# Kernel tuning notes

Hardware: AMD Instinct MI355X
Metric: run time of the kernel (lower is better)

## Reference

```python
import jax, jax.numpy as jnp
import numpy as np

B, L, HS = 2, 2048, 2048
NH, NKV, HD = 16, 4, 128
EPS = 1e-6
ROPE_BASE = 10000.0
SCALE = HD ** -0.5


def setup_inputs() -> dict:
    key = jax.random.key(0)
    ks = jax.random.split(key, 5)
    w = lambda k, shape: (jax.random.normal(k, shape, jnp.float32) * 0.02)
    return {
        "hidden_states": jax.random.normal(ks[0], (B, L, HS), jnp.float32),
        "Wq": w(ks[1], (HS, NH * HD)),
        "Wk": w(ks[2], (HS, NKV * HD)),
        "Wv": w(ks[3], (HS, NKV * HD)),
        "Wo": w(ks[4], (NH * HD, HS)),
        "q_norm_w": jnp.ones((HD,), jnp.float32),
        "k_norm_w": jnp.ones((HD,), jnp.float32),
    }


def _rmsnorm(x, w):
    return x * jax.lax.rsqrt(jnp.mean(x * x, axis=-1, keepdims=True) + EPS) * w


def _rope(x, cos, sin):
    # x: [B, L, heads, HD]; cos/sin: [1, L, 1, HD//2]
    x1, x2 = jnp.split(x, 2, axis=-1)
    return jnp.concatenate([x1 * cos - x2 * sin, x2 * cos + x1 * sin], axis=-1)


def reference(hidden_states, Wq, Wk, Wv, Wo, q_norm_w, k_norm_w):
    b, l, _ = hidden_states.shape
    n_rep = NH // NKV
    q = (hidden_states @ Wq).reshape(b, l, NH, HD)
    k = (hidden_states @ Wk).reshape(b, l, NKV, HD)
    v = (hidden_states @ Wv).reshape(b, l, NKV, HD)
    # QK RMSNorm over head_dim
    q = _rmsnorm(q, q_norm_w)
    k = _rmsnorm(k, k_norm_w)
    # RoPE with position_ids = arange(L)
    pos = jnp.arange(l, dtype=jnp.float32)
    inv_freq = 1.0 / (ROPE_BASE ** (jnp.arange(0, HD, 2, dtype=jnp.float32) / HD))
    ang = pos[:, None] * inv_freq  # [L, HD//2]
    cos = jnp.cos(ang)[None, :, None, :]
    sin = jnp.sin(ang)[None, :, None, :]
    q = _rope(q, cos, sin)
    k = _rope(k, cos, sin)
    # GQA: torch expand+reshape gives q head h -> kv head (h mod NKV);
    # reshape q to [B, L, n_rep, NKV, HD] (h = r*NKV + j) and contract per kv group.
    qg = q.reshape(b, l, n_rep, NKV, HD)
    scores = jnp.einsum("blrjd,bmjd->brjlm", qg, k) * SCALE  # [B, r, j, L, L]
    causal = jnp.tril(jnp.ones((l, l), dtype=bool))
    scores = jnp.where(causal, scores, -jnp.inf)
    probs = jax.nn.softmax(scores, axis=-1)
    out = jnp.einsum("brjlm,bmjd->blrjd", probs, v).reshape(b, l, NH * HD)
    return out @ Wo
```

## Files before the change

kernel.cpp:

```cpp
#include <hip/hip_runtime.h>
#include <hip/hip_bf16.h>

#define B_  2
#define L_  2048
#define HS_ 2048
#define NH_ 16
#define NKV_ 4
#define HD_ 128
#define EPS_ 1e-6f
#define SCALE_ 0.08838834764831843f
#define LOG2E_ 1.4426950408889634f

typedef __attribute__((ext_vector_type(8))) short bf16x8;
typedef __attribute__((ext_vector_type(4))) float f32x4;

__device__ __forceinline__ f32x4 mfma16(bf16x8 a, bf16x8 b, f32x4 c) {
    return __builtin_amdgcn_mfma_f32_16x16x32_bf16(a, b, c, 0, 0, 0);
}

__device__ __forceinline__ void async_copy16(void* lds, const void* g) {
    __builtin_amdgcn_global_load_lds(
        (const __attribute__((address_space(1))) unsigned int*)g,
        (__attribute__((address_space(3))) unsigned int*)lds,
        16, 0, 0);
}

__device__ __forceinline__ unsigned cvtpk(float lo, float hi) {
    unsigned r;
    asm("v_cvt_pk_bf16_f32 %0, %1, %2" : "=v"(r) : "v"(lo), "v"(hi));
    return r;
}

__global__ __launch_bounds__(256) void cvt_f32_bf16(const float* __restrict__ src,
                                                    __hip_bfloat16* __restrict__ dst,
                                                    int n4) {
    int i = blockIdx.x * 256 + threadIdx.x;
    if (i >= n4) return;
    float4 v = ((const float4*)src)[i];
    union { __hip_bfloat16 h[4]; short4 s; } u;
    u.h[0] = __float2bfloat16(v.x);
    u.h[1] = __float2bfloat16(v.y);
    u.h[2] = __float2bfloat16(v.z);
    u.h[3] = __float2bfloat16(v.w);
    ((short4*)dst)[i] = u.s;
}

__global__ __launch_bounds__(256) void transpose_cvt(const float* __restrict__ src,
                                                     __hip_bfloat16* __restrict__ dst,
                                                     int K, int N) {
    __shared__ float tile[32][33];
    int n0 = blockIdx.x * 32, k0 = blockIdx.y * 32;
    int tx = threadIdx.x & 31, ty = threadIdx.x >> 5;
#pragma unroll
    for (int i = 0; i < 32; i += 8)
        tile[ty + i][tx] = src[(size_t)(k0 + ty + i) * N + n0 + tx];
    __syncthreads();
#pragma unroll
    for (int i = 0; i < 32; i += 8)
        dst[(size_t)(n0 + ty + i) * K + k0 + tx] = __float2bfloat16(tile[tx][ty + i]);
}

__global__ __launch_bounds__(256) void v_transpose(const float* __restrict__ KV,
                                                   __hip_bfloat16* __restrict__ Vt) {
    __shared__ float tile[32][33];
    int bkv = blockIdx.z;
    int b = bkv >> 2, kv = bkv & 3;
    int l0 = blockIdx.x * 32, d0 = blockIdx.y * 32;
    int tx = threadIdx.x & 31, ty = threadIdx.x >> 5;
#pragma unroll
    for (int i = 0; i < 32; i += 8)
        tile[ty + i][tx] = KV[(size_t)(b * L_ + l0 + ty + i) * 1024 + 512 + kv * HD_ + d0 + tx];
    __syncthreads();
#pragma unroll
    for (int i = 0; i < 32; i += 8)
        Vt[((size_t)(b * NKV_ + kv) * HD_ + d0 + ty + i) * L_ + l0 + tx] =
            __float2bfloat16(tile[tx][ty + i]);
}

#define GNT 32
#define GKB 4096
__global__ __launch_bounds__(512, 2) void gemm8_bf16(const __hip_bfloat16* __restrict__ A,
                                                     const __hip_bfloat16* __restrict__ Bt,
                                                     float* __restrict__ C1,
                                                     float* __restrict__ C2,
                                                     int Ntot, int splitN) {
    __shared__ __align__(16) char lds[131072];
    int t = threadIdx.x;
    int w = t >> 6, lane = t & 63;
    int row16 = lane & 15, quad = lane >> 4, e7 = row16 & 7;
    int wr = w >> 2, wc = w & 3;

    int gx = gridDim.x;
    int nwg = gx * gridDim.y;
    int bid = blockIdx.y * gx + blockIdx.x;
    int cpx = nwg >> 3;
    int swz = (bid & 7) * cpx + (bid >> 3);
    int bx = swz % gx, by = swz / gx;
    int m0 = bx * 256, n0 = by * 256;

    const char* baseA[2];
    const char* baseB[2];
#pragma unroll
    for (int kc = 0; kc < 2; ++kc) {
        int so = ((kc * 4 + quad) ^ e7) << 4;
        baseA[kc] = lds + wr * 16384 + row16 * 128 + so;
        baseB[kc] = lds + 65536 + wc * 8192 + row16 * 128 + so;
    }

    int r8 = lane >> 3;
    int sl = (lane & 7) ^ r8;
    char* dstA = lds + wr * 16384 + (w & 3) * 2048 + lane * 16;
    char* dstB = lds + 65536 + (w >> 1) * 8192 + (w & 1) * 2048 + lane * 16;
    const char* gA = (const char*)A +
        (size_t)(m0 + wr * 128 + (w & 3) * 16 + r8) * GKB + sl * 16;
    const char* gB = (const char*)Bt +
        (size_t)(n0 + (w >> 1) * 64 + (w & 1) * 16 + r8) * GKB + sl * 16;

    f32x4 acc[8][4] = {};
    bf16x8 a[4][2], b[2][2];

#pragma unroll
    for (int i = 0; i < 2; ++i) async_copy16(dstA + i * 1024, gA + i * 32768);
#pragma unroll
    for (int i = 0; i < 2; ++i) async_copy16(dstB + i * 1024, gB + i * 32768);
#pragma unroll
    for (int i = 0; i < 2; ++i) async_copy16(dstB + 4096 + i * 1024, gB + 131072 + i * 32768);
#pragma unroll
    for (int i = 0; i < 2; ++i) async_copy16(dstA + 8192 + i * 1024, gA + 262144 + i * 32768);

    for (int Tb = 0; Tb < GNT; Tb += 2) {
#pragma unroll
        for (int u = 0; u < 2; ++u) {
            const int T = Tb + u;
            const int cu = u * 32768, du = (u ^ 1) * 32768;
            const int tn = (T + 1 < GNT ? T + 1 : T) * 128;

            asm volatile("s_waitcnt vmcnt(4)" ::: "memory");
            __builtin_amdgcn_s_barrier();
            __builtin_amdgcn_sched_barrier(0);
#pragma unroll
            for (int mi = 0; mi < 4; ++mi)
#pragma unroll
                for (int kc = 0; kc < 2; ++kc)
                    a[mi][kc] = *(const bf16x8*)(baseA[kc] + cu + mi * 2048);
#pragma unroll
            for (int ni = 0; ni < 2; ++ni)
#pragma unroll
                for (int kc = 0; kc < 2; ++kc)
                    b[ni][kc] = *(const bf16x8*)(baseB[kc] + cu + ni * 2048);
#pragma unroll
            for (int i = 0; i < 2; ++i)
                async_copy16(dstA + du + i * 1024, gA + tn + i * 32768);
            asm volatile("s_waitcnt lgkmcnt(0)" ::: "memory");
            __builtin_amdgcn_sched_barrier(0);
            __builtin_amdgcn_s_setprio(1);
#pragma unroll
            for (int mi = 0; mi < 4; ++mi)
#pragma unroll
                for (int ni = 0; ni < 2; ++ni)
#pragma unroll
                    for (int kc = 0; kc < 2; ++kc)
                        acc[mi][ni] = mfma16(a[mi][kc], b[ni][kc], acc[mi][ni]);
            __builtin_amdgcn_s_setprio(0);

            asm volatile("s_waitcnt vmcnt(4)" ::: "memory");
            __builtin_amdgcn_s_barrier();
            __builtin_amdgcn_sched_barrier(0);
#pragma unroll
            for (int ni = 0; ni < 2; ++ni)
#pragma unroll
                for (int kc = 0; kc < 2; ++kc)
                    b[ni][kc] = *(const bf16x8*)(baseB[kc] + cu + 4096 + ni * 2048);
#pragma unroll
            for (int i = 0; i < 2; ++i)
                async_copy16(dstB + du + i * 1024, gB + tn + i * 32768);
            asm volatile("s_waitcnt lgkmcnt(0)" ::: "memory");
            __builtin_amdgcn_sched_barrier(0);
            __builtin_amdgcn_s_setprio(1);
#pragma unroll
            for (int mi = 0; mi < 4; ++mi)
#pragma unroll
                for (int ni = 0; ni < 2; ++ni)
#pragma unroll
                    for (int kc = 0; kc < 2; ++kc)
                        acc[mi][2 + ni] = mfma16(a[mi][kc], b[ni][kc], acc[mi][2 + ni]);
            __builtin_amdgcn_s_setprio(0);

            asm volatile("s_waitcnt vmcnt(4)" ::: "memory");
            __builtin_amdgcn_s_barrier();
            __builtin_amdgcn_sched_barrier(0);
#pragma unroll
            for (int mi = 0; mi < 4; ++mi)
#pragma unroll
                for (int kc = 0; kc < 2; ++kc)
                    a[mi][kc] = *(const bf16x8*)(baseA[kc] + cu + 8192 + mi * 2048);
#pragma unroll
            for (int i = 0; i < 2; ++i)
                async_copy16(dstB + du + 4096 + i * 1024, gB + 131072 + tn + i * 32768);
            asm volatile("s_waitcnt lgkmcnt(0)" ::: "memory");
            __builtin_amdgcn_sched_barrier(0);
            __builtin_amdgcn_s_setprio(1);
#pragma unroll
            for (int mi = 0; mi < 4; ++mi)
#pragma unroll
                for (int ni = 0; ni < 2; ++ni)
#pragma unroll
                    for (int kc = 0; kc < 2; ++kc)
                        acc[4 + mi][2 + ni] = mfma16(a[mi][kc], b[ni][kc], acc[4 + mi][2 + ni]);
            __builtin_amdgcn_s_setprio(0);

            __builtin_amdgcn_s_barrier();
            __builtin_amdgcn_sched_barrier(0);
#pragma unroll
            for (int ni = 0; ni < 2; ++ni)
#pragma unroll
                for (int kc = 0; kc < 2; ++kc)
                    b[ni][kc] = *(const bf16x8*)(baseB[kc] + cu + ni * 2048);
#pragma unroll
            for (int i = 0; i < 2; ++i)
                async_copy16(dstA + du + 8192 + i * 1024, gA + 262144 + tn + i * 32768);
            asm volatile("s_waitcnt lgkmcnt(0)" ::: "memory");
            __builtin_amdgcn_sched_barrier(0);
            __builtin_amdgcn_s_setprio(1);
#pragma unroll
            for (int mi = 0; mi < 4; ++mi)
#pragma unroll
                for (int ni = 0; ni < 2; ++ni)
#pragma unroll
                    for (int kc = 0; kc < 2; ++kc)
                        acc[4 + mi][ni] = mfma16(a[mi][kc], b[ni][kc], acc[4 + mi][ni]);
            __builtin_amdgcn_s_setprio(0);
        }
    }

    float* Cb; int cs, ccol0;
    if (n0 < splitN) { Cb = C1; cs = splitN; ccol0 = n0; }
    else             { Cb = C2; cs = Ntot - splitN; ccol0 = n0 - splitN; }
#pragma unroll
    for (int mi = 0; mi < 8; ++mi)
#pragma unroll
        for (int ni = 0; ni < 4; ++ni) {
            int rbase = m0 + wr * 128 + mi * 16 + quad * 4;
            int col = ccol0 + wc * 64 + ni * 16 + row16;
#pragma unroll
            for (int r = 0; r < 4; ++r)
                Cb[(size_t)(rbase + r) * cs + col] = acc[mi][ni][r];
        }
}

__global__ __launch_bounds__(512, 2) void gemm_o(const __hip_bfloat16* __restrict__ A,
                                                 const __hip_bfloat16* __restrict__ Bt,
                                                 float* __restrict__ C) {
    __shared__ __align__(16) char lds[98304];
    int t = threadIdx.x;
    int w = t >> 6, lane = t & 63;
    int row16 = lane & 15, quad = lane >> 4, e7 = row16 & 15 & 7;
    int wr = w >> 2, wc = w & 3;

    int gx = gridDim.x;
    int nwg = gx * gridDim.y;
    int bid = blockIdx.y * gx + blockIdx.x;
    int cpx = nwg >> 3;
    int swz = (bid & 7) * cpx + (bid >> 3);
    int bx = swz % gx, by = swz / gx;
    int m0 = bx * 128, n0 = by * 256;

    const char* baseA[2];
    const char* baseB[2];
#pragma unroll
    for (int kc = 0; kc < 2; ++kc) {
        int so = ((kc * 4 + quad) ^ e7) << 4;
        baseA[kc] = lds + wr * 8192 + row16 * 128 + so;
        baseB[kc] = lds + 32768 + wc * 8192 + row16 * 128 + so;
    }

    int r8 = lane >> 3;
    int sl = (lane & 7) ^ r8;
    int arow_lo = ((w & 4) << 4) + (w & 3) * 8;
    int li0 = w * 2;
    int brow_lo0 = ((li0) >> 2) * 64 + ((li0) & 3) * 8;
    int brow_lo1 = ((li0 + 1) >> 2) * 64 + ((li0 + 1) & 3) * 8;

    char* dAlo = lds + arow_lo * 128 + lane * 16;
    char* dBlo0 = lds + 32768 + brow_lo0 * 128 + lane * 16;
    char* dBlo1 = lds + 32768 + brow_lo1 * 128 + lane * 16;
    const char* gAlo = (const char*)A + (size_t)(m0 + arow_lo + r8) * GKB + sl * 16;
    const char* gBlo0 = (const char*)Bt + (size_t)(n0 + brow_lo0 + r8) * GKB + sl * 16;
    const char* gBlo1 = (const char*)Bt + (size_t)(n0 + brow_lo1 + r8) * GKB + sl * 16;
    const int HI_L = 32 * 128;
    const size_t HI_G = (size_t)32 * GKB;

    f32x4 acc[4][4] = {};
    bf16x8 a[2][2], b[2][2];

    async_copy16(dAlo, gAlo);
    async_copy16(dBlo0, gBlo0);
    async_copy16(dBlo1, gBlo1);
    async_copy16(dBlo0 + HI_L, gBlo0 + HI_G);
    async_copy16(dBlo1 + HI_L, gBlo1 + HI_G);
    async_copy16(dAlo + HI_L, gAlo + HI_G);

    for (int Tb = 0; Tb < GNT; Tb += 2) {
#pragma unroll
        for (int u = 0; u < 2; ++u) {
            const int T = Tb + u;
            const int cuA = u * 16384, duA = (u ^ 1) * 16384;
            const int cuB = u * 32768, duB = (u ^ 1) * 32768;
            const int tn = (T + 1 < GNT ? T + 1 : T) * 128;

            asm volatile("s_waitcnt vmcnt(3)" ::: "memory");
            __builtin_amdgcn_s_barrier();
            __builtin_amdgcn_sched_barrier(0);
#pragma unroll
            for (int mi = 0; mi < 2; ++mi)
#pragma unroll
                for (int kc = 0; kc < 2; ++kc)
                    a[mi][kc] = *(const bf16x8*)(baseA[kc] + cuA + mi * 2048);
#pragma unroll
            for (int ni = 0; ni < 2; ++ni)
#pragma unroll
                for (int kc = 0; kc < 2; ++kc)
                    b[ni][kc] = *(const bf16x8*)(baseB[kc] + cuB + ni * 2048);
            async_copy16(dAlo + duA, gAlo + tn);
            asm volatile("s_waitcnt lgkmcnt(0)" ::: "memory");
            __builtin_amdgcn_sched_barrier(0);
            __builtin_amdgcn_s_setprio(1);
#pragma unroll
            for (int mi = 0; mi < 2; ++mi)
#pragma unroll
                for (int ni = 0; ni < 2; ++ni)
#pragma unroll
                    for (int kc = 0; kc < 2; ++kc)
                        acc[mi][ni] = mfma16(a[mi][kc], b[ni][kc], acc[mi][ni]);
            __builtin_amdgcn_s_setprio(0);

            asm volatile("s_waitcnt vmcnt(2)" ::: "memory");
            __builtin_amdgcn_s_barrier();
            __builtin_amdgcn_sched_barrier(0);
#pragma unroll
            for (int ni = 0; ni < 2; ++ni)
#pragma unroll
                for (int kc = 0; kc < 2; ++kc)
                    b[ni][kc] = *(const bf16x8*)(baseB[kc] + cuB + 4096 + ni * 2048);
            async_copy16(dBlo0 + duB, gBlo0 + tn);
            async_copy16(dBlo1 + duB, gBlo1 + tn);
            asm volatile("s_waitcnt lgkmcnt(0)" ::: "memory");
            __builtin_amdgcn_sched_barrier(0);
            __builtin_amdgcn_s_setprio(1);
#pragma unroll
            for (int mi = 0; mi < 2; ++mi)
#pragma unroll
                for (int ni = 0; ni < 2; ++ni)
#pragma unroll
                    for (int kc = 0; kc < 2; ++kc)
                        acc[mi][2 + ni] = mfma16(a[mi][kc], b[ni][kc], acc[mi][2 + ni]);
            __builtin_amdgcn_s_setprio(0);

            asm volatile("s_waitcnt vmcnt(3)" ::: "memory");
            __builtin_amdgcn_s_barrier();
            __builtin_amdgcn_sched_barrier(0);
#pragma unroll
            for (int mi = 0; mi < 2; ++mi)
#pragma unroll
                for (int kc = 0; kc < 2; ++kc)
                    a[mi][kc] = *(const bf16x8*)(baseA[kc] + cuA + 4096 + mi * 2048);
            async_copy16(dBlo0 + HI_L + duB, gBlo0 + HI_G + tn);
            async_copy16(dBlo1 + HI_L + duB, gBlo1 + HI_G + tn);
            asm volatile("s_waitcnt lgkmcnt(0)" ::: "memory");
            __builtin_amdgcn_sched_barrier(0);
            __builtin_amdgcn_s_setprio(1);
#pragma unroll
            for (int mi = 0; mi < 2; ++mi)
#pragma unroll
                for (int ni = 0; ni < 2; ++ni)
#pragma unroll
                    for (int kc = 0; kc < 2; ++kc)
                        acc[2 + mi][2 + ni] = mfma16(a[mi][kc], b[ni][kc], acc[2 + mi][2 + ni]);
            __builtin_amdgcn_s_setprio(0);

            __builtin_amdgcn_s_barrier();
            __builtin_amdgcn_sched_barrier(0);
#pragma unroll
            for (int ni = 0; ni < 2; ++ni)
#pragma unroll
                for (int kc = 0; kc < 2; ++kc)
                    b[ni][kc] = *(const bf16x8*)(baseB[kc] + cuB + ni * 2048);
            async_copy16(dAlo + HI_L + duA, gAlo + HI_G + tn);
            asm volatile("s_waitcnt lgkmcnt(0)" ::: "memory");
            __builtin_amdgcn_sched_barrier(0);
            __builtin_amdgcn_s_setprio(1);
#pragma unroll
            for (int mi = 0; mi < 2; ++mi)
#pragma unroll
                for (int ni = 0; ni < 2; ++ni)
#pragma unroll
                    for (int kc = 0; kc < 2; ++kc)
                        acc[2 + mi][ni] = mfma16(a[mi][kc], b[ni][kc], acc[2 + mi][ni]);
            __builtin_amdgcn_s_setprio(0);
        }
    }
    asm volatile("s_waitcnt vmcnt(0)" ::: "memory");

#pragma unroll
    for (int mi = 0; mi < 4; ++mi)
#pragma unroll
        for (int ni = 0; ni < 4; ++ni) {
            int rbase = m0 + wr * 64 + mi * 16 + quad * 4;
            int col = n0 + wc * 64 + ni * 16 + row16;
#pragma unroll
            for (int r = 0; r < 4; ++r)
                C[(size_t)(rbase + r) * 2048 + col] = acc[mi][ni][r];
        }
}

__global__ __launch_bounds__(256) void norm_rope(const float* __restrict__ X,
                                                 __hip_bfloat16* __restrict__ Y,
                                                 const float* __restrict__ w,
                                                 int log2nh, int in_stride, float oscale) {
    int row = blockIdx.x * 4 + (threadIdx.x >> 6);
    int lane = threadIdx.x & 63;
    int m = row >> log2nh;
    int head = row & ((1 << log2nh) - 1);
    int pos = m & (L_ - 1);
    const float* x = X + (size_t)m * in_stride + head * HD_;
    float x1 = x[lane], x2 = x[lane + 64];
    float ss = x1 * x1 + x2 * x2;
#pragma unroll
    for (int mm = 1; mm < 64; mm <<= 1) ss += __shfl_xor(ss, mm);
    float rms = rsqrtf(ss * (1.0f / 128.0f) + EPS_);
    float xn1 = x1 * rms * w[lane];
    float xn2 = x2 * rms * w[lane + 64];
    float inv_freq = __builtin_exp2f(-(float)lane * 0.20762050593046014f);
    float ang = (float)pos * inv_freq;
    float c = cosf(ang), s = sinf(ang);
    __hip_bfloat16* y = Y + (size_t)row * HD_;
    y[lane]      = __float2bfloat16((xn1 * c - xn2 * s) * oscale);
    y[lane + 64] = __float2bfloat16((xn2 * c + xn1 * s) * oscale);
}

__global__ __launch_bounds__(256, 2) void flash_attn(const __hip_bfloat16* __restrict__ Q,
                                                     const __hip_bfloat16* __restrict__ Kb,
                                                     const __hip_bfloat16* __restrict__ Vt,
                                                     __hip_bfloat16* __restrict__ O) {
    __shared__ __align__(16) __hip_bfloat16 sK[2][64 * 128];
    __shared__ __align__(16) __hip_bfloat16 sV[2][128 * 64];
    __shared__ __align__(16) __hip_bfloat16 sP[4][16 * 72];

    int t = threadIdx.x, wave = t >> 6, lane = t & 63;
    int row16 = lane & 15, quad = lane >> 4;
    int h = blockIdx.y, b = blockIdx.z;
    int kv = h & (NKV_ - 1);
    int x = blockIdx.x;
    int qtA = x, qtB = 31 - x;
    int nA = qtA + 1;
    const int nTot = 33;

    int e7 = row16 & 7;
    int kOff[4], vOff[2];
#pragma unroll
    for (int kc = 0; kc < 4; ++kc)
        kOff[kc] = row16 * 256 + (((kc * 4 + quad) ^ e7) * 16);
#pragma unroll
    for (int kc2 = 0; kc2 < 2; ++kc2)
        vOff[kc2] = row16 * 128 + (((kc2 * 4 + quad) ^ e7) * 16);

    const char* sKb = (const char*)&sK[0][0];
    const char* sVb = (const char*)&sV[0][0];
    char* myP = (char*)&sP[wave][0];
    int pW = row16 * 144 + quad * 8;
    int pR = row16 * 144 + quad * 16;

    const char* gK[4];
    const char* gV[4];
#pragma unroll
    for (int i = 0; i < 4; ++i) {
        int rk = wave * 16 + i * 4 + quad;
        int ck = row16 ^ (rk & 7);
        gK[i] = (const char*)(Kb + ((size_t)(b * L_ + rk) * NKV_ + kv) * HD_ + ck * 8);
        int rv = wave * 32 + i * 8 + (lane >> 3);
        int cv = (lane & 7) ^ (rv & 7);
        gV[i] = (const char*)(Vt + ((size_t)(b * NKV_ + kv) * HD_ + rv) * L_ + cv * 8);
    }
    char* dK = (char*)&sK[0][0] + wave * 4096 + lane * 16;
    char* dV = (char*)&sV[0][0] + wave * 4096 + lane * 16;

    bf16x8 qf[4];
    f32x4 accO[8];
    float lrow;
    int q0w = 0;

    auto loadQ = [&](int qt) {
        q0w = qt * 64 + wave * 16;
        const __hip_bfloat16* qbase =
            Q + ((size_t)(b * L_ + q0w + row16) * NH_ + h) * HD_ + quad * 8;
#pragma unroll
        for (int kc = 0; kc < 4; ++kc) qf[kc] = *(const bf16x8*)(qbase + kc * 32);
#pragma unroll
        for (int db = 0; db < 8; ++db) accO[db] = f32x4{0.f, 0.f, 0.f, 0.f};
        lrow = 0.f;
    };

    auto epilogue = [&]() {
        float l = lrow;
        l += __shfl_xor(l, 16);
        l += __shfl_xor(l, 32);
        float linv = 1.0f / l;
        __hip_bfloat16* obase = O + ((size_t)(b * L_ + q0w + row16) * NH_ + h) * HD_;
#pragma unroll
        for (int db = 0; db < 8; ++db) {
            union { __hip_bfloat16 h4[4]; short4 s4; } u;
#pragma unroll
            for (int r = 0; r < 4; ++r) u.h4[r] = __float2bfloat16(accO[db][r] * linv);
            *(short4*)(obase + db * 16 + quad * 4) = u.s4;
        }
    };

    auto stage = [&](int s1) {
        int kb64 = (s1 < nA ? s1 : s1 - nA) * 64;
        int buf = (s1 & 1) * 16384;
        int ko = kb64 * 1024;
        int vo = kb64 * 2;
#pragma unroll
        for (int i = 0; i < 4; ++i) {
            async_copy16(dK + buf + i * 1024, gK[i] + ko);
            async_copy16(dV + buf + i * 1024, gV[i] + vo);
        }
    };

    loadQ(qtA);
    stage(0);
    for (int s = 0; s < nTot; ++s) {
        __syncthreads();
        if (s + 1 < nTot) stage(s + 1);
        if (s == nA) { epilogue(); loadQ(qtB); }
        int kcur = (s < nA ? s : s - nA) * 64;
        const char* cK = sKb + (s & 1) * 16384;
        const char* cV = sVb + (s & 1) * 16384;

        f32x4 st[4];
        __builtin_amdgcn_s_setprio(1);
#pragma unroll
        for (int kb = 0; kb < 4; ++kb) {
            f32x4 acc = {};
#pragma unroll
            for (int kc = 0; kc < 4; ++kc) {
                bf16x8 kf = *(const bf16x8*)(cK + kb * 4096 + kOff[kc]);
                acc = mfma16(kf, qf[kc], acc);
            }
            st[kb] = acc;
        }
        __builtin_amdgcn_s_setprio(0);

        float p[4][4];
        if (kcur + 63 > q0w) {
            int qgRel = q0w + row16 - kcur - quad * 4;
#pragma unroll
            for (int kb = 0; kb < 4; ++kb)
#pragma unroll
                for (int r = 0; r < 4; ++r) {
                    float e = __builtin_exp2f(st[kb][r]);
                    p[kb][r] = (kb * 16 + r <= qgRel) ? e : 0.f;
                }
        } else {
#pragma unroll
            for (int kb = 0; kb < 4; ++kb)
#pragma unroll
                for (int r = 0; r < 4; ++r)
                    p[kb][r] = __builtin_exp2f(st[kb][r]);
        }
#pragma unroll
        for (int kb = 0; kb < 4; ++kb)
#pragma unroll
            for (int r = 0; r < 4; ++r) lrow += p[kb][r];

#pragma unroll
        for (int kb = 0; kb < 4; ++kb) {
            uint2 u;
            u.x = cvtpk(p[kb][0], p[kb][1]);
            u.y = cvtpk(p[kb][2], p[kb][3]);
            *(uint2*)(myP + pW + kb * 32) = u;
        }
        asm volatile("s_waitcnt lgkmcnt(0)" ::: "memory");
        bf16x8 pf[2];
        pf[0] = *(const bf16x8*)(myP + pR);
        pf[1] = *(const bf16x8*)(myP + pR + 64);

        __builtin_amdgcn_s_setprio(1);
#pragma unroll
        for (int db = 0; db < 8; ++db) {
#pragma unroll
            for (int kc2 = 0; kc2 < 2; ++kc2) {
                bf16x8 vf = *(const bf16x8*)(cV + db * 2048 + vOff[kc2]);
                accO[db] = mfma16(vf, pf[kc2], accO[db]);
            }
        }
        __builtin_amdgcn_s_setprio(0);
    }
    epilogue();
}

extern "C" void kernel_launch(void* const* d_in, const int* in_sizes, int n_in,
                              void* d_out, int out_size, void* d_ws, size_t ws_size,
                              hipStream_t stream) {
    const float* hidden = (const float*)d_in[0];
    const float* Wq = (const float*)d_in[1];
    const float* Wk = (const float*)d_in[2];
    const float* Wv = (const float*)d_in[3];
    const float* Wo = (const float*)d_in[4];
    const float* qw = (const float*)d_in[5];
    const float* kw = (const float*)d_in[6];
    float* out = (float*)d_out;

    char* ws = (char*)d_ws;
    size_t off = 0;
    auto alloc = [&](size_t bytes) { char* p = ws + off; off += (bytes + 255) & ~255ull; return p; };
    __hip_bfloat16* Wq_t = (__hip_bfloat16*)alloc((size_t)HS_ * NH_ * HD_ * 2);
    __hip_bfloat16* Wk_t = (__hip_bfloat16*)alloc((size_t)HS_ * NKV_ * HD_ * 2);
    __hip_bfloat16* Wv_t = (__hip_bfloat16*)alloc((size_t)HS_ * NKV_ * HD_ * 2);
    __hip_bfloat16* Wo_t = (__hip_bfloat16*)alloc((size_t)HS_ * NH_ * HD_ * 2);
    __hip_bfloat16* A_h  = (__hip_bfloat16*)alloc((size_t)B_ * L_ * HS_ * 2);
    float* kv_f32 = (float*)alloc((size_t)B_ * L_ * 1024 * 4);
    __hip_bfloat16* q_bf  = (__hip_bfloat16*)alloc((size_t)B_ * L_ * NH_ * HD_ * 2);
    __hip_bfloat16* k_bf  = (__hip_bfloat16*)alloc((size_t)B_ * L_ * NKV_ * HD_ * 2);
    __hip_bfloat16* vt_bf = (__hip_bfloat16*)alloc((size_t)B_ * NKV_ * HD_ * L_ * 2);
    float* q_f32 = out;
    __hip_bfloat16* attn_bf = A_h;

    const int M = B_ * L_;

    cvt_f32_bf16<<<(M * HS_ / 4 + 255) / 256, 256, 0, stream>>>(hidden, A_h, M * HS_ / 4);
    transpose_cvt<<<dim3(2048 / 32, 2048 / 32), 256, 0, stream>>>(Wq, Wq_t, HS_, 2048);
    transpose_cvt<<<dim3(512 / 32, 2048 / 32), 256, 0, stream>>>(Wk, Wk_t, HS_, 512);
    transpose_cvt<<<dim3(512 / 32, 2048 / 32), 256, 0, stream>>>(Wv, Wv_t, HS_, 512);
    transpose_cvt<<<dim3(2048 / 32, 2048 / 32), 256, 0, stream>>>(Wo, Wo_t, HS_, 2048);
    gemm8_bf16<<<dim3(M / 256, 3072 / 256), 512, 0, stream>>>(
        A_h, Wq_t, q_f32, kv_f32, 3072, 2048);
    norm_rope<<<(M * NH_) / 4, 256, 0, stream>>>(q_f32, q_bf, qw, 4, 2048, SCALE_ * LOG2E_);
    norm_rope<<<(M * NKV_) / 4, 256, 0, stream>>>(kv_f32, k_bf, kw, 2, 1024, 1.0f);
    v_transpose<<<dim3(L_ / 32, HD_ / 32, B_ * NKV_), 256, 0, stream>>>(kv_f32, vt_bf);
    flash_attn<<<dim3(16, NH_, B_), 256, 0, stream>>>(q_bf, k_bf, vt_bf, attn_bf);
    gemm_o<<<dim3(M / 128, 2048 / 256), 512, 0, stream>>>(attn_bf, Wo_t, out);
}
```

Baseline: 303.7 us.

## Process two 16-row query groups per wave in flash attention with 128-thread blocks

Each wave now handles 32 query rows (two 16-row MFMA groups) instead of 16, and the block shrinks from four waves to two while keeping a 64-row query tile. K and V fragments read from LDS are reused across both query groups, halving LDS read traffic per MFMA. Each wave issues twice as many async K/V copies to fill the same tiles. The cost is doubled accumulator registers per thread and fewer resident waves per CU for latency hiding.

New measurement: 321.3 us. 5.8% more time.

```diff
diff --git a/kernel.cpp b/kernel.cpp
--- a/kernel.cpp
+++ b/kernel.cpp
@@ -438,13 +438,13 @@
     y[lane + 64] = __float2bfloat16((xn2 * c + xn1 * s) * oscale);
 }
 
-__global__ __launch_bounds__(256, 2) void flash_attn(const __hip_bfloat16* __restrict__ Q,
+__global__ __launch_bounds__(128, 1) void flash_attn(const __hip_bfloat16* __restrict__ Q,
                                                      const __hip_bfloat16* __restrict__ Kb,
                                                      const __hip_bfloat16* __restrict__ Vt,
                                                      __hip_bfloat16* __restrict__ O) {
     __shared__ __align__(16) __hip_bfloat16 sK[2][64 * 128];
     __shared__ __align__(16) __hip_bfloat16 sV[2][128 * 64];
-    __shared__ __align__(16) __hip_bfloat16 sP[4][16 * 72];
+    __shared__ __align__(16) __hip_bfloat16 sP[2][16 * 72];
 
     int t = threadIdx.x, wave = t >> 6, lane = t & 63;
     int row16 = lane & 15, quad = lane >> 4;
@@ -470,48 +470,55 @@
     int pW = row16 * 144 + quad * 8;
     int pR = row16 * 144 + quad * 16;
 
-    const char* gK[4];
-    const char* gV[4];
-#pragma unroll
-    for (int i = 0; i < 4; ++i) {
-        int rk = wave * 16 + i * 4 + quad;
+    const char* gK[8];
+    const char* gV[8];
+#pragma unroll
+    for (int i = 0; i < 8; ++i) {
+        int rk = wave * 32 + i * 4 + quad;
         int ck = row16 ^ (rk & 7);
         gK[i] = (const char*)(Kb + ((size_t)(b * L_ + rk) * NKV_ + kv) * HD_ + ck * 8);
-        int rv = wave * 32 + i * 8 + (lane >> 3);
+        int rv = wave * 64 + i * 8 + (lane >> 3);
         int cv = (lane & 7) ^ (rv & 7);
         gV[i] = (const char*)(Vt + ((size_t)(b * NKV_ + kv) * HD_ + rv) * L_ + cv * 8);
     }
-    char* dK = (char*)&sK[0][0] + wave * 4096 + lane * 16;
-    char* dV = (char*)&sV[0][0] + wave * 4096 + lane * 16;
-
-    bf16x8 qf[4];
-    f32x4 accO[8];
-    float lrow;
+    char* dK = (char*)&sK[0][0] + wave * 8192 + lane * 16;
+    char* dV = (char*)&sV[0][0] + wave * 8192 + lane * 16;
+
+    bf16x8 qf[2][4];
+    f32x4 accO[2][8];
+    float lrow[2];
     int q0w = 0;
 
     auto loadQ = [&](int qt) {
-        q0w = qt * 64 + wave * 16;
-        const __hip_bfloat16* qbase =
-            Q + ((size_t)(b * L_ + q0w + row16) * NH_ + h) * HD_ + quad * 8;
-#pragma unroll
-        for (int kc = 0; kc < 4; ++kc) qf[kc] = *(const bf16x8*)(qbase + kc * 32);
-#pragma unroll
-        for (int db = 0; db < 8; ++db) accO[db] = f32x4{0.f, 0.f, 0.f, 0.f};
-        lrow = 0.f;
+        q0w = qt * 64 + wave * 32;
+#pragma unroll
+        for (int qg = 0; qg < 2; ++qg) {
+            const __hip_bfloat16* qbase =
+                Q + ((size_t)(b * L_ + q0w + qg * 16 + row16) * NH_ + h) * HD_ + quad * 8;
+#pragma unroll
+            for (int kc = 0; kc < 4; ++kc) qf[qg][kc] = *(const bf16x8*)(qbase + kc * 32);
+#pragma unroll
+            for (int db = 0; db < 8; ++db) accO[qg][db] = f32x4{0.f, 0.f, 0.f, 0.f};
+            lrow[qg] = 0.f;
+        }
     };
 
     auto epilogue = [&]() {
-        float l = lrow;
-        l += __shfl_xor(l, 16);
-        l += __shfl_xor(l, 32);
-        float linv = 1.0f / l;
-        __hip_bfloat16* obase = O + ((size_t)(b * L_ + q0w + row16) * NH_ + h) * HD_;
-#pragma unroll
-        for (int db = 0; db < 8; ++db) {
-            union { __hip_bfloat16 h4[4]; short4 s4; } u;
-#pragma unroll
-            for (int r = 0; r < 4; ++r) u.h4[r] = __float2bfloat16(accO[db][r] * linv);
-            *(short4*)(obase + db * 16 + quad * 4) = u.s4;
+#pragma unroll
+        for (int qg = 0; qg < 2; ++qg) {
+            float l = lrow[qg];
+            l += __shfl_xor(l, 16);
+            l += __shfl_xor(l, 32);
+            float linv = 1.0f / l;
+            __hip_bfloat16* obase =
+                O + ((size_t)(b * L_ + q0w + qg * 16 + row16) * NH_ + h) * HD_;
+#pragma unroll
+            for (int db = 0; db < 8; ++db) {
+                union { __hip_bfloat16 h4[4]; short4 s4; } u;
+#pragma unroll
+                for (int r = 0; r < 4; ++r) u.h4[r] = __float2bfloat16(accO[qg][db][r] * linv);
+                *(short4*)(obase + db * 16 + quad * 4) = u.s4;
+            }
         }
     };
 
@@ -521,7 +528,7 @@
         int ko = kb64 * 1024;
         int vo = kb64 * 2;
 #pragma unroll
-        for (int i = 0; i < 4; ++i) {
+        for (int i = 0; i < 8; ++i) {
             async_copy16(dK + buf + i * 1024, gK[i] + ko);
             async_copy16(dV + buf + i * 1024, gV[i] + vo);
         }
@@ -537,53 +544,75 @@
         const char* cK = sKb + (s & 1) * 16384;
         const char* cV = sVb + (s & 1) * 16384;
 
-        f32x4 st[4];
+        f32x4 st[2][4];
         __builtin_amdgcn_s_setprio(1);
 #pragma unroll
         for (int kb = 0; kb < 4; ++kb) {
-            f32x4 acc = {};
-#pragma unroll
-            for (int kc = 0; kc < 4; ++kc) {
-                bf16x8 kf = *(const bf16x8*)(cK + kb * 4096 + kOff[kc]);
-                acc = mfma16(kf, qf[kc], acc);
+            bf16x8 kf[4];
+#pragma unroll
+            for (int kc = 0; kc < 4; ++kc)
+                kf[kc] = *(const bf16x8*)(cK + kb * 4096 + kOff[kc]);
+#pragma unroll
+            for (int qg = 0; qg < 2; ++qg) {
+                f32x4 acc = {};
+#pragma unroll
+                for (int kc = 0; kc < 4; ++kc)
+                    acc = mfma16(kf[kc], qf[qg][kc], acc);
+                st[qg][kb] = acc;
             }
-            st[kb] = acc;
         }
         __builtin_amdgcn_s_setprio(0);
 
-        float p[4][4];
+        float p[2][4][4];
         if (kcur + 63 > q0w) {
-            int qgRel = q0w + row16 - kcur - quad * 4;
+#pragma unroll
+            for (int qg = 0; qg < 2; ++qg) {
+                int qgRel = q0w + qg * 16 + row16 - kcur - quad * 4;
+#pragma unroll
+                for (int kb = 0; kb < 4; ++kb)
+#pragma unroll
+                    for (int r = 0; r < 4; ++r) {
+                        float e = __builtin_exp2f(st[qg][kb][r]);
+                        p[qg][kb][r] = (kb * 16 + r <= qgRel) ? e : 0.f;
+                    }
+            }
+        } else {
+#pragma unroll
+            for (int qg = 0; qg < 2; ++qg)
+#pragma unroll
+                for (int kb = 0; kb < 4; ++kb)
+#pragma unroll
+                    for (int r = 0; r < 4; ++r)
+                        p[qg][kb][r] = __builtin_exp2f(st[qg][kb][r]);
+        }
+#pragma unroll
+        for (int qg = 0; qg < 2; ++qg)
 #pragma unroll
             for (int kb = 0; kb < 4; ++kb)
 #pragma unroll
-                for (int r = 0; r < 4; ++r) {
-                    float e = __builtin_exp2f(st[kb][r]);
-                    p[kb][r] = (kb * 16 + r <= qgRel) ? e : 0.f;
-                }
-        } else {
-#pragma unroll
-            for (int kb = 0; kb < 4; ++kb)
-#pragma unroll
-                for (int r = 0; r < 4; ++r)
-                    p[kb][r] = __builtin_exp2f(st[kb][r]);
-        }
-#pragma unroll
-        for (int kb = 0; kb < 4; ++kb)
-#pragma unroll
-            for (int r = 0; r < 4; ++r) lrow += p[kb][r];
-
+                for (int r = 0; r < 4; ++r) lrow[qg] += p[qg][kb][r];
+
+        bf16x8 pf0[2], pf1[2];
 #pragma unroll
         for (int kb = 0; kb < 4; ++kb) {
             uint2 u;
-            u.x = cvtpk(p[kb][0], p[kb][1]);
-            u.y = cvtpk(p[kb][2], p[kb][3]);
+            u.x = cvtpk(p[0][kb][0], p[0][kb][1]);
+            u.y = cvtpk(p[0][kb][2], p[0][kb][3]);
             *(uint2*)(myP + pW + kb * 32) = u;
         }
         asm volatile("s_waitcnt lgkmcnt(0)" ::: "memory");
-        bf16x8 pf[2];
-        pf[0] = *(const bf16x8*)(myP + pR);
-        pf[1] = *(const bf16x8*)(myP + pR + 64);
+        pf0[0] = *(const bf16x8*)(myP + pR);
+        pf0[1] = *(const bf16x8*)(myP + pR + 64);
+#pragma unroll
+        for (int kb = 0; kb < 4; ++kb) {
+            uint2 u;
+            u.x = cvtpk(p[1][kb][0], p[1][kb][1]);
+            u.y = cvtpk(p[1][kb][2], p[1][kb][3]);
+            *(uint2*)(myP + pW + kb * 32) = u;
+        }
+        asm volatile("s_waitcnt lgkmcnt(0)" ::: "memory");
+        pf1[0] = *(const bf16x8*)(myP + pR);
+        pf1[1] = *(const bf16x8*)(myP + pR + 64);
 
         __builtin_amdgcn_s_setprio(1);
 #pragma unroll
@@ -591,7 +620,8 @@
 #pragma unroll
             for (int kc2 = 0; kc2 < 2; ++kc2) {
                 bf16x8 vf = *(const bf16x8*)(cV + db * 2048 + vOff[kc2]);
-                accO[db] = mfma16(vf, pf[kc2], accO[db]);
+                accO[0][db] = mfma16(vf, pf0[kc2], accO[0][db]);
+                accO[1][db] = mfma16(vf, pf1[kc2], accO[1][db]);
             }
         }
         __builtin_amdgcn_s_setprio(0);
@@ -638,6 +668,6 @@
     norm_rope<<<(M * NH_) / 4, 256, 0, stream>>>(q_f32, q_bf, qw, 4, 2048, SCALE_ * LOG2E_);
     norm_rope<<<(M * NKV_) / 4, 256, 0, stream>>>(kv_f32, k_bf, kw, 2, 1024, 1.0f);
     v_transpose<<<dim3(L_ / 32, HD_ / 32, B_ * NKV_), 256, 0, stream>>>(kv_f32, vt_bf);
-    flash_attn<<<dim3(16, NH_, B_), 256, 0, stream>>>(q_bf, k_bf, vt_bf, attn_bf);
+    flash_attn<<<dim3(16, NH_, B_), 128, 0, stream>>>(q_bf, k_bf, vt_bf, attn_bf);
     gemm_o<<<dim3(M / 128, 2048 / 256), 512, 0, stream>>>(attn_bf, Wo_t, out);
 }
```
